# Kernel optimization log

Hardware: AMD Instinct MI355X
Metric: run time of the kernel (lower is better)

## Reference

```python
import jax, jax.numpy as jnp
import numpy as np

NUM_USERS = 150000
NUM_ITEMS = 80000
N_NODES = NUM_USERS + NUM_ITEMS
NNZ = 5000000
LATENT_DIM = 64
N_LAYERS = 3


def setup_inputs() -> dict:
    key = jax.random.key(0)
    k1, k2, k3, k4, k5 = jax.random.split(key, 5)
    user_emb = 0.1 * jax.random.normal(k1, (NUM_USERS, LATENT_DIM), dtype=jnp.float32)
    item_emb = 0.1 * jax.random.normal(k2, (NUM_ITEMS, LATENT_DIM), dtype=jnp.float32)
    adj_rows = jax.random.randint(k3, (NNZ,), 0, N_NODES, dtype=jnp.int32)
    adj_cols = jax.random.randint(k4, (NNZ,), 0, N_NODES, dtype=jnp.int32)
    # scale values ~ 1/avg_degree so propagation is stable (mimics sym-normalized adjacency)
    adj_vals = jax.random.uniform(k5, (NNZ,), dtype=jnp.float32) * (N_NODES / NNZ)
    return {"user_emb": user_emb, "item_emb": item_emb,
            "adj_rows": adj_rows, "adj_cols": adj_cols, "adj_vals": adj_vals}


def _spmm(rows, cols, vals, x):
    # y[r] = sum_{e: rows[e]==r} vals[e] * x[cols[e]]  == torch.sparse.mm(G, x)
    return jax.ops.segment_sum(vals[:, None] * x[cols], rows, num_segments=N_NODES)


def reference(user_emb, item_emb, adj_rows, adj_cols, adj_vals):
    all_emb = jnp.concatenate([user_emb, item_emb], axis=0)  # [N, d]
    acc = all_emb
    for _ in range(N_LAYERS):
        all_emb = _spmm(adj_rows, adj_cols, adj_vals, all_emb)
        acc = acc + all_emb
    light_out = acc / (N_LAYERS + 1)  # mean over stacked layer embeddings
    users = light_out[:NUM_USERS]
    items = light_out[NUM_USERS:]
    return users, items
```

## Files before the change

### kernel.cpp

```cpp
#include <hip/hip_runtime.h>

#define NUM_USERS 150000
#define NUM_ITEMS 80000
#define N_NODES   230000
#define NNZ       5000000
#define DIM       64

#define SB_SHIFT 10
#define SB_SIZE  1024
#define NUM_SB   ((N_NODES + SB_SIZE - 1) / SB_SIZE)
#define SB_CAP   32768
#define PA_ITEMS 4

#define DBINS 256

#define VAL_MAX   0.046f
#define VAL_ENC   (16384.0f / VAL_MAX)
#define VAL_SCALE (VAL_MAX / 16384.0f)

__device__ __forceinline__ float bf2f(unsigned short h) {
    return __uint_as_float(((unsigned int)h) << 16);
}
__device__ __forceinline__ unsigned short f2bf(float f) {
    unsigned int u = __float_as_uint(f);
    u += 0x7FFFu + ((u >> 16) & 1u);
    return (unsigned short)(u >> 16);
}
__device__ __forceinline__ float bflo(unsigned int u) {
    return __uint_as_float(u << 16);
}
__device__ __forceinline__ float bfhi(unsigned int u) {
    return __uint_as_float(u & 0xFFFF0000u);
}
__device__ __forceinline__ unsigned int pk2(float a, float b) {
    return (unsigned int)f2bf(a) | ((unsigned int)f2bf(b) << 16);
}

__global__ void init_kernel(const float* __restrict__ u,
                            const float* __restrict__ it,
                            unsigned short* __restrict__ x) {
    long i = (long)blockIdx.x * blockDim.x + threadIdx.x;
    const long n4  = (long)N_NODES * DIM / 4;
    const long iu4 = (long)NUM_USERS * DIM / 4;
    if (i >= n4) return;
    float4 v = (i < iu4) ? ((const float4*)u)[i]
                         : ((const float4*)it)[i - iu4];
    ushort4 h;
    h.x = f2bf(v.x); h.y = f2bf(v.y); h.z = f2bf(v.z); h.w = f2bf(v.w);
    ((ushort4*)x)[i] = h;
}

__global__ void cursor_init_kernel(int* __restrict__ bucket_cursor,
                                   int* __restrict__ dhist) {
    int t = threadIdx.x;
    if (t < NUM_SB) bucket_cursor[t] = t * SB_CAP;
    dhist[t] = 0;
}

__global__ void partA_kernel(const int* __restrict__ rows,
                             const int* __restrict__ cols,
                             const float* __restrict__ vals,
                             int* __restrict__ bucket_cursor,
                             unsigned int* __restrict__ Xe,
                             unsigned short* __restrict__ Xr) {
    __shared__ int bcnt[NUM_SB];
    __shared__ int bbase[NUM_SB];
    const int t = threadIdx.x;
    const long tile = 1024L * PA_ITEMS;
    for (long base = (long)blockIdx.x * tile; base < NNZ;
         base += (long)gridDim.x * tile) {
        for (int j = t; j < NUM_SB; j += 1024) bcnt[j] = 0;
        __syncthreads();
        int b[PA_ITEMS], rank[PA_ITEMS], rl[PA_ITEMS];
        unsigned int pk[PA_ITEMS];
        bool ok[PA_ITEMS];
        for (int k = 0; k < PA_ITEMS; ++k) {
            long e = base + (long)k * 1024 + t;
            ok[k] = (e < NNZ);
            if (ok[k]) {
                int r = rows[e];
                b[k]  = r >> SB_SHIFT;
                rl[k] = r & (SB_SIZE - 1);
                int vc = (int)(vals[e] * VAL_ENC + 0.5f);
                vc = min(vc, 16383);
                pk[k] = ((unsigned int)vc << 18) | (unsigned int)cols[e];
                rank[k] = atomicAdd(&bcnt[b[k]], 1);
            }
        }
        __syncthreads();
        for (int j = t; j < NUM_SB; j += 1024)
            if (bcnt[j] > 0) bbase[j] = atomicAdd(&bucket_cursor[j], bcnt[j]);
        __syncthreads();
        for (int k = 0; k < PA_ITEMS; ++k)
            if (ok[k]) {
                int pos = bbase[b[k]] + rank[k];
                Xe[pos] = pk[k];
                Xr[pos] = (unsigned short)rl[k];
            }
        __syncthreads();
    }
}

__global__ void sb_scan_kernel(const int* __restrict__ bucket_cursor,
                               int* __restrict__ sb_base) {
    __shared__ int lds[256];
    const int t = threadIdx.x;
    const int s = (t < NUM_SB) ? (bucket_cursor[t] - t * SB_CAP) : 0;
    lds[t] = s;
    __syncthreads();
    for (int off = 1; off < 256; off <<= 1) {
        int add = (t >= off) ? lds[t - off] : 0;
        __syncthreads();
        lds[t] += add;
        __syncthreads();
    }
    if (t < NUM_SB) sb_base[t] = lds[t] - s;
    if (t == 0) sb_base[NUM_SB] = NNZ;
}

__global__ void partB_kernel(const unsigned int* __restrict__ Xe,
                             const unsigned short* __restrict__ Xr,
                             const int* __restrict__ sb_base,
                             int* __restrict__ row_start,
                             unsigned int* __restrict__ edges) {
    __shared__ int hist[SB_SIZE];
    __shared__ int scan[SB_SIZE];
    const int b    = blockIdx.x;
    const int t    = threadIdx.x;
    const int rlo  = b << SB_SHIFT;
    const int nrows = min(SB_SIZE, N_NODES - rlo);
    const int xoff = b * SB_CAP;
    const int base = sb_base[b];
    const int cnt  = sb_base[b + 1] - base;
    hist[t] = 0;
    __syncthreads();
    for (int i = t; i < cnt; i += 1024)
        atomicAdd(&hist[Xr[xoff + i]], 1);
    __syncthreads();
    const int v = hist[t];
    scan[t] = v;
    __syncthreads();
    for (int off = 1; off < 1024; off <<= 1) {
        int add = (t >= off) ? scan[t - off] : 0;
        __syncthreads();
        scan[t] += add;
        __syncthreads();
    }
    const int rs = base + (scan[t] - v);
    if (t < nrows) row_start[rlo + t] = rs;
    hist[t] = rs;
    __syncthreads();
    for (int i = t; i < cnt; i += 1024) {
        int rl = Xr[xoff + i];
        int pos = atomicAdd(&hist[rl], 1);
        edges[pos] = Xe[xoff + i];
    }
    if (b == 0 && t == 0) row_start[N_NODES] = NNZ;
}

__global__ void deg_hist_kernel(const int* __restrict__ row_start,
                                int* __restrict__ dhist) {
    __shared__ int h[DBINS];
    const int t = threadIdx.x;
    h[t] = 0;
    __syncthreads();
    int r = blockIdx.x * 256 + t;
    if (r < N_NODES) {
        int d = row_start[r + 1] - row_start[r];
        atomicAdd(&h[min(d, DBINS - 1)], 1);
    }
    __syncthreads();
    if (h[t]) atomicAdd(&dhist[t], h[t]);
}

__global__ void deg_scan_kernel(const int* __restrict__ dhist,
                                int* __restrict__ dcur) {
    __shared__ int lds[DBINS];
    const int t = threadIdx.x;
    const int s = dhist[t];
    lds[t] = s;
    __syncthreads();
    for (int off = 1; off < DBINS; off <<= 1) {
        int add = (t >= off) ? lds[t - off] : 0;
        __syncthreads();
        lds[t] += add;
        __syncthreads();
    }
    dcur[t] = lds[t] - s;
}

__global__ void deg_scatter_kernel(const int* __restrict__ row_start,
                                   int* __restrict__ dcur,
                                   uint4* __restrict__ desc) {
    __shared__ int bcnt[DBINS];
    __shared__ int bbase[DBINS];
    const int t = threadIdx.x;
    bcnt[t] = 0;
    __syncthreads();
    int r = blockIdx.x * 256 + t;
    int bin = 0, rank = 0, s = 0, d = 0;
    const bool ok = (r < N_NODES);
    if (ok) {
        s = row_start[r];
        d = row_start[r + 1] - s;
        bin = min(d, DBINS - 1);
        rank = atomicAdd(&bcnt[bin], 1);
    }
    __syncthreads();
    if (bcnt[t]) bbase[t] = atomicAdd(&dcur[t], bcnt[t]);
    __syncthreads();
    if (ok)
        desc[bbase[bin] + rank] =
            make_uint4((unsigned)r, (unsigned)s, (unsigned)d, 0u);
}

#define FMA8(v, h) \
    a0 = fmaf((v), bflo((h).x), a0); a1 = fmaf((v), bfhi((h).x), a1); \
    a2 = fmaf((v), bflo((h).y), a2); a3 = fmaf((v), bfhi((h).y), a3); \
    a4 = fmaf((v), bflo((h).z), a4); a5 = fmaf((v), bfhi((h).z), a5); \
    a6 = fmaf((v), bflo((h).w), a6); a7 = fmaf((v), bfhi((h).w), a7);

__global__ __launch_bounds__(256)
void spmm8_kernel(const uint4* __restrict__ desc,
                  const unsigned int* __restrict__ edges,
                  const unsigned short* __restrict__ x,
                  unsigned short* __restrict__ y) {
    const int lane = threadIdx.x & 63;
    const int oct  = lane >> 3;
    const int fo   = (lane & 7) << 3;
    const long wv  = (long)blockIdx.x * 4 + (threadIdx.x >> 6);
    const long rowIdx = wv * 8 + oct;
    const bool valid = (rowIdx < N_NODES);
    const uint4 dsc = desc[valid ? rowIdx : (N_NODES - 1)];
    const int r = (int)dsc.x;
    const int s = (int)dsc.y;
    const int deg = valid ? (int)dsc.z : 0;
    int dm = deg;
    dm = max(dm, __shfl_xor(dm, 8));
    dm = max(dm, __shfl_xor(dm, 16));
    dm = max(dm, __shfl_xor(dm, 32));
    dm = __builtin_amdgcn_readfirstlane(dm);
    const unsigned short* xf = x + fo;
    float a0 = 0, a1 = 0, a2 = 0, a3 = 0, a4 = 0, a5 = 0, a6 = 0, a7 = 0;
    for (int i = 0; i < dm; i += 2) {
        const int o0 = (i     < deg) ? (s + i)     : 0;
        const int o1 = (i + 1 < deg) ? (s + i + 1) : 0;
        const unsigned int e0 = edges[o0];
        const unsigned int e1 = edges[o1];
        const uint4 ha = *(const uint4*)(xf + (((long)(e0 & 0x3FFFF)) << 6));
        const uint4 hb = *(const uint4*)(xf + (((long)(e1 & 0x3FFFF)) << 6));
        const float v0 = (i     < deg) ? (float)(e0 >> 18) * VAL_SCALE : 0.0f;
        const float v1 = (i + 1 < deg) ? (float)(e1 >> 18) * VAL_SCALE : 0.0f;
        FMA8(v0, ha);
        FMA8(v1, hb);
    }
    if (valid) {
        uint4 w;
        w.x = pk2(a0, a1); w.y = pk2(a2, a3);
        w.z = pk2(a4, a5); w.w = pk2(a6, a7);
        *(uint4*)(y + (((long)r) << 6) + fo) = w;
    }
}

__global__ __launch_bounds__(256)
void spmm_final8_kernel(const uint4* __restrict__ desc,
                        const unsigned int* __restrict__ edges,
                        const unsigned short* __restrict__ y2,
                        const unsigned short* __restrict__ y1,
                        const float* __restrict__ u,
                        const float* __restrict__ it,
                        float* __restrict__ acc) {
    const int lane = threadIdx.x & 63;
    const int oct  = lane >> 3;
    const int fo   = (lane & 7) << 3;
    const long wv  = (long)blockIdx.x * 4 + (threadIdx.x >> 6);
    const long rowIdx = wv * 8 + oct;
    const bool valid = (rowIdx < N_NODES);
    const uint4 dsc = desc[valid ? rowIdx : (N_NODES - 1)];
    const int r = (int)dsc.x;
    const int s = (int)dsc.y;
    const int deg = valid ? (int)dsc.z : 0;
    int dm = deg;
    dm = max(dm, __shfl_xor(dm, 8));
    dm = max(dm, __shfl_xor(dm, 16));
    dm = max(dm, __shfl_xor(dm, 32));
    dm = __builtin_amdgcn_readfirstlane(dm);
    const unsigned short* xf = y2 + fo;
    float a0 = 0, a1 = 0, a2 = 0, a3 = 0, a4 = 0, a5 = 0, a6 = 0, a7 = 0;
    for (int i = 0; i < dm; i += 2) {
        const int o0 = (i     < deg) ? (s + i)     : 0;
        const int o1 = (i + 1 < deg) ? (s + i + 1) : 0;
        const unsigned int e0 = edges[o0];
        const unsigned int e1 = edges[o1];
        const uint4 ha = *(const uint4*)(xf + (((long)(e0 & 0x3FFFF)) << 6));
        const uint4 hb = *(const uint4*)(xf + (((long)(e1 & 0x3FFFF)) << 6));
        const float v0 = (i     < deg) ? (float)(e0 >> 18) * VAL_SCALE : 0.0f;
        const float v1 = (i + 1 < deg) ? (float)(e1 >> 18) * VAL_SCALE : 0.0f;
        FMA8(v0, ha);
        FMA8(v1, hb);
    }
    if (valid) {
        const long o = (((long)r) << 6) + fo;
        const float* x0p = (r < NUM_USERS) ? (u + o)
                         : (it + o - (((long)NUM_USERS) << 6));
        const float4 xa = *(const float4*)(x0p);
        const float4 xb = *(const float4*)(x0p + 4);
        const uint4 h1 = *(const uint4*)(y1 + o);
        const uint4 h2 = *(const uint4*)(y2 + o);
        float4 ra, rb;
        ra.x = (xa.x + bflo(h1.x) + bflo(h2.x) + a0) * 0.25f;
        ra.y = (xa.y + bfhi(h1.x) + bfhi(h2.x) + a1) * 0.25f;
        ra.z = (xa.z + bflo(h1.y) + bflo(h2.y) + a2) * 0.25f;
        ra.w = (xa.w + bfhi(h1.y) + bfhi(h2.y) + a3) * 0.25f;
        rb.x = (xb.x + bflo(h1.z) + bflo(h2.z) + a4) * 0.25f;
        rb.y = (xb.y + bfhi(h1.z) + bfhi(h2.z) + a5) * 0.25f;
        rb.z = (xb.z + bflo(h1.w) + bflo(h2.w) + a6) * 0.25f;
        rb.w = (xb.w + bfhi(h1.w) + bfhi(h2.w) + a7) * 0.25f;
        *(float4*)(acc + o) = ra;
        *(float4*)(acc + o + 4) = rb;
    }
}

extern "C" void kernel_launch(void* const* d_in, const int* in_sizes, int n_in,
                              void* d_out, int out_size, void* d_ws, size_t ws_size,
                              hipStream_t stream) {
    const float* u    = (const float*)d_in[0];
    const float* it   = (const float*)d_in[1];
    const int*   rows = (const int*)d_in[2];
    const int*   cols = (const int*)d_in[3];
    const float* vals = (const float*)d_in[4];
    float* acc = (float*)d_out;

    const size_t bufBf = (size_t)N_NODES * DIM * 2;
    const size_t edgeB = (size_t)NNZ * 4;
    const size_t XeB   = (size_t)NUM_SB * SB_CAP * 4;
    const size_t XrB   = (size_t)NUM_SB * SB_CAP * 2;
    const size_t nodeB = 921600;
    char* ws = (char*)d_ws;
    unsigned short* buf0 = (unsigned short*)(ws);
    unsigned short* buf1 = (unsigned short*)(ws + bufBf);
    unsigned short* buf2 = (unsigned short*)(ws + 2 * bufBf);
    unsigned int*   edges = (unsigned int*)(ws + 3 * bufBf);
    unsigned int*   Xe   = (unsigned int*)(ws + 3 * bufBf + edgeB);
    unsigned short* Xr   = (unsigned short*)(ws + 3 * bufBf + edgeB + XeB);
    char* p              = ws + 3 * bufBf + edgeB + XeB + XrB;
    int* row_start       = (int*)(p);   p += nodeB;
    int* bucket_cursor   = (int*)(p);   p += 1024;
    int* sb_base         = (int*)(p);   p += 1024;
    int* dhist           = (int*)(p);   p += DBINS * 4;
    int* dcur            = (int*)(p);
    uint4* desc          = (uint4*)Xe;

    const int n4 = N_NODES * DIM / 4;
    const int ewGrid = (n4 + 255) / 256;
    const int rowBlocks = (N_NODES + 255) / 256;

    init_kernel<<<ewGrid, 256, 0, stream>>>(u, it, buf0);

    cursor_init_kernel<<<1, 256, 0, stream>>>(bucket_cursor, dhist);
    partA_kernel<<<512, 1024, 0, stream>>>(rows, cols, vals, bucket_cursor, Xe, Xr);
    sb_scan_kernel<<<1, 256, 0, stream>>>(bucket_cursor, sb_base);
    partB_kernel<<<NUM_SB, 1024, 0, stream>>>(Xe, Xr, sb_base, row_start, edges);

    deg_hist_kernel<<<rowBlocks, 256, 0, stream>>>(row_start, dhist);
    deg_scan_kernel<<<1, DBINS, 0, stream>>>(dhist, dcur);
    deg_scatter_kernel<<<rowBlocks, 256, 0, stream>>>(row_start, dcur, desc);

    const long waves = (N_NODES + 7) / 8;
    const int spmmGrid = (int)((waves + 3) / 4);
    spmm8_kernel<<<spmmGrid, 256, 0, stream>>>(desc, edges, buf0, buf1);
    spmm8_kernel<<<spmmGrid, 256, 0, stream>>>(desc, edges, buf1, buf2);
    spmm_final8_kernel<<<spmmGrid, 256, 0, stream>>>(desc, edges, buf2,
                                                     buf1, u, it, acc);
}
```

Before: 604.0 us.

## Sort edges by column segment within rows and unroll SpMM gathers by four

The partition kernel now bins each row's edges into eight column segments using a per-row, per-segment LDS histogram, so edges within a row are ordered roughly by source column. This aims to improve L2 locality of the gathered embedding rows across concurrent waves. The SpMM kernels also unroll the edge loop to four gathers per iteration and use nontemporal loads for the edge stream to keep it from polluting cache. The cost is eight times more LDS in the partition kernel and more registers per thread in the SpMM kernels.

```diff
diff --git a/kernel.cpp b/kernel.cpp
--- a/kernel.cpp
+++ b/kernel.cpp
@@ -11,6 +11,9 @@
 #define NUM_SB   ((N_NODES + SB_SIZE - 1) / SB_SIZE)
 #define SB_CAP   32768
 #define PA_ITEMS 4
+
+#define SEG_SHIFT 15
+#define NSEG      8
 
 #define DBINS 256
 
@@ -123,8 +126,8 @@
                              const int* __restrict__ sb_base,
                              int* __restrict__ row_start,
                              unsigned int* __restrict__ edges) {
-    __shared__ int hist[SB_SIZE];
-    __shared__ int scan[SB_SIZE];
+    __shared__ int hist[SB_SIZE * NSEG];
+    __shared__ int rsum[SB_SIZE];
     const int b    = blockIdx.x;
     const int t    = threadIdx.x;
     const int rlo  = b << SB_SHIFT;
@@ -132,28 +135,38 @@
     const int xoff = b * SB_CAP;
     const int base = sb_base[b];
     const int cnt  = sb_base[b + 1] - base;
-    hist[t] = 0;
-    __syncthreads();
-    for (int i = t; i < cnt; i += 1024)
-        atomicAdd(&hist[Xr[xoff + i]], 1);
-    __syncthreads();
-    const int v = hist[t];
-    scan[t] = v;
+    for (int j = t; j < SB_SIZE * NSEG; j += 1024) hist[j] = 0;
+    __syncthreads();
+    for (int i = t; i < cnt; i += 1024) {
+        const unsigned int pk = Xe[xoff + i];
+        const int rl  = Xr[xoff + i];
+        const int seg = (int)((pk & 0x3FFFFu) >> SEG_SHIFT);
+        atomicAdd(&hist[(rl << 3) | seg], 1);
+    }
+    __syncthreads();
+    int c[NSEG]; int tot = 0;
+    #pragma unroll
+    for (int k = 0; k < NSEG; ++k) { c[k] = hist[(t << 3) | k]; tot += c[k]; }
+    rsum[t] = tot;
     __syncthreads();
     for (int off = 1; off < 1024; off <<= 1) {
-        int add = (t >= off) ? scan[t - off] : 0;
-        __syncthreads();
-        scan[t] += add;
-        __syncthreads();
-    }
-    const int rs = base + (scan[t] - v);
+        int add = (t >= off) ? rsum[t - off] : 0;
+        __syncthreads();
+        rsum[t] += add;
+        __syncthreads();
+    }
+    const int rs = base + (rsum[t] - tot);
     if (t < nrows) row_start[rlo + t] = rs;
-    hist[t] = rs;
+    int run = rs;
+    #pragma unroll
+    for (int k = 0; k < NSEG; ++k) { int tmp = c[k]; hist[(t << 3) | k] = run; run += tmp; }
     __syncthreads();
     for (int i = t; i < cnt; i += 1024) {
-        int rl = Xr[xoff + i];
-        int pos = atomicAdd(&hist[rl], 1);
-        edges[pos] = Xe[xoff + i];
+        const unsigned int pk = Xe[xoff + i];
+        const int rl  = Xr[xoff + i];
+        const int seg = (int)((pk & 0x3FFFFu) >> SEG_SHIFT);
+        const int pos = atomicAdd(&hist[(rl << 3) | seg], 1);
+        edges[pos] = pk;
     }
     if (b == 0 && t == 0) row_start[N_NODES] = NNZ;
 }
@@ -242,17 +255,27 @@
     dm = __builtin_amdgcn_readfirstlane(dm);
     const unsigned short* xf = x + fo;
     float a0 = 0, a1 = 0, a2 = 0, a3 = 0, a4 = 0, a5 = 0, a6 = 0, a7 = 0;
-    for (int i = 0; i < dm; i += 2) {
+    for (int i = 0; i < dm; i += 4) {
         const int o0 = (i     < deg) ? (s + i)     : 0;
         const int o1 = (i + 1 < deg) ? (s + i + 1) : 0;
-        const unsigned int e0 = edges[o0];
-        const unsigned int e1 = edges[o1];
+        const int o2 = (i + 2 < deg) ? (s + i + 2) : 0;
+        const int o3 = (i + 3 < deg) ? (s + i + 3) : 0;
+        const unsigned int e0 = __builtin_nontemporal_load(edges + o0);
+        const unsigned int e1 = __builtin_nontemporal_load(edges + o1);
+        const unsigned int e2 = __builtin_nontemporal_load(edges + o2);
+        const unsigned int e3 = __builtin_nontemporal_load(edges + o3);
         const uint4 ha = *(const uint4*)(xf + (((long)(e0 & 0x3FFFF)) << 6));
         const uint4 hb = *(const uint4*)(xf + (((long)(e1 & 0x3FFFF)) << 6));
+        const uint4 hc = *(const uint4*)(xf + (((long)(e2 & 0x3FFFF)) << 6));
+        const uint4 hd = *(const uint4*)(xf + (((long)(e3 & 0x3FFFF)) << 6));
         const float v0 = (i     < deg) ? (float)(e0 >> 18) * VAL_SCALE : 0.0f;
         const float v1 = (i + 1 < deg) ? (float)(e1 >> 18) * VAL_SCALE : 0.0f;
+        const float v2 = (i + 2 < deg) ? (float)(e2 >> 18) * VAL_SCALE : 0.0f;
+        const float v3 = (i + 3 < deg) ? (float)(e3 >> 18) * VAL_SCALE : 0.0f;
         FMA8(v0, ha);
         FMA8(v1, hb);
+        FMA8(v2, hc);
+        FMA8(v3, hd);
     }
     if (valid) {
         uint4 w;
@@ -287,17 +310,27 @@
     dm = __builtin_amdgcn_readfirstlane(dm);
     const unsigned short* xf = y2 + fo;
     float a0 = 0, a1 = 0, a2 = 0, a3 = 0, a4 = 0, a5 = 0, a6 = 0, a7 = 0;
-    for (int i = 0; i < dm; i += 2) {
+    for (int i = 0; i < dm; i += 4) {
         const int o0 = (i     < deg) ? (s + i)     : 0;
         const int o1 = (i + 1 < deg) ? (s + i + 1) : 0;
-        const unsigned int e0 = edges[o0];
-        const unsigned int e1 = edges[o1];
+        const int o2 = (i + 2 < deg) ? (s + i + 2) : 0;
+        const int o3 = (i + 3 < deg) ? (s + i + 3) : 0;
+        const unsigned int e0 = __builtin_nontemporal_load(edges + o0);
+        const unsigned int e1 = __builtin_nontemporal_load(edges + o1);
+        const unsigned int e2 = __builtin_nontemporal_load(edges + o2);
+        const unsigned int e3 = __builtin_nontemporal_load(edges + o3);
         const uint4 ha = *(const uint4*)(xf + (((long)(e0 & 0x3FFFF)) << 6));
         const uint4 hb = *(const uint4*)(xf + (((long)(e1 & 0x3FFFF)) << 6));
+        const uint4 hc = *(const uint4*)(xf + (((long)(e2 & 0x3FFFF)) << 6));
+        const uint4 hd = *(const uint4*)(xf + (((long)(e3 & 0x3FFFF)) << 6));
         const float v0 = (i     < deg) ? (float)(e0 >> 18) * VAL_SCALE : 0.0f;
         const float v1 = (i + 1 < deg) ? (float)(e1 >> 18) * VAL_SCALE : 0.0f;
+        const float v2 = (i + 2 < deg) ? (float)(e2 >> 18) * VAL_SCALE : 0.0f;
+        const float v3 = (i + 3 < deg) ? (float)(e3 >> 18) * VAL_SCALE : 0.0f;
         FMA8(v0, ha);
         FMA8(v1, hb);
+        FMA8(v2, hc);
+        FMA8(v3, hd);
     }
     if (valid) {
         const long o = (((long)r) << 6) + fo;
```

Result: slower. 657.3 us (+8.8%).

## Build sliced-ELL edge layout with global atomic scatter instead of two-pass bucket sort

Applied to the files above, without the earlier changes.

Replaces the two-pass bucket sort (partA/partB) that built CSR with a per-row count histogram plus degree-sorted slices of 8 rows. Each slice is padded to a multiple of 4 and its edges are interleaved, so the SpMM loop drops per-lane degree predicates and reads 4 edges per iteration. Edges are placed by a global atomic scatter, and padded slots are zero-filled so they contribute nothing. The cost is extra small kernels, a zero-fill of the padded edge buffer, and heavy global atomic traffic in the scatter, in exchange for a simpler, branch-free inner loop.

```diff
diff --git a/kernel.cpp b/kernel.cpp
--- a/kernel.cpp
+++ b/kernel.cpp
@@ -6,11 +6,9 @@
 #define NNZ       5000000
 #define DIM       64
 
-#define SB_SHIFT 10
-#define SB_SIZE  1024
-#define NUM_SB   ((N_NODES + SB_SIZE - 1) / SB_SIZE)
-#define SB_CAP   32768
-#define PA_ITEMS 4
+#define NSLICES   ((N_NODES + 7) / 8)
+#define SCAN_BLKS ((NSLICES + 1023) / 1024)
+#define ECAP      6000000
 
 #define DBINS 256
 
@@ -18,9 +16,6 @@
 #define VAL_ENC   (16384.0f / VAL_MAX)
 #define VAL_SCALE (VAL_MAX / 16384.0f)
 
-__device__ __forceinline__ float bf2f(unsigned short h) {
-    return __uint_as_float(((unsigned int)h) << 16);
-}
 __device__ __forceinline__ unsigned short f2bf(float f) {
     unsigned int u = __float_as_uint(f);
     u += 0x7FFFu + ((u >> 16) & 1u);
@@ -38,8 +33,12 @@
 
 __global__ void init_kernel(const float* __restrict__ u,
                             const float* __restrict__ it,
-                            unsigned short* __restrict__ x) {
+                            unsigned short* __restrict__ x,
+                            int* __restrict__ row_cnt,
+                            int* __restrict__ dhist) {
     long i = (long)blockIdx.x * blockDim.x + threadIdx.x;
+    if (i < N_NODES) row_cnt[i] = 0;
+    if (i < DBINS) dhist[i] = 0;
     const long n4  = (long)N_NODES * DIM / 4;
     const long iu4 = (long)NUM_USERS * DIM / 4;
     if (i >= n4) return;
@@ -50,125 +49,30 @@
     ((ushort4*)x)[i] = h;
 }
 
-__global__ void cursor_init_kernel(int* __restrict__ bucket_cursor,
-                                   int* __restrict__ dhist) {
-    int t = threadIdx.x;
-    if (t < NUM_SB) bucket_cursor[t] = t * SB_CAP;
-    dhist[t] = 0;
-}
-
-__global__ void partA_kernel(const int* __restrict__ rows,
-                             const int* __restrict__ cols,
-                             const float* __restrict__ vals,
-                             int* __restrict__ bucket_cursor,
-                             unsigned int* __restrict__ Xe,
-                             unsigned short* __restrict__ Xr) {
-    __shared__ int bcnt[NUM_SB];
-    __shared__ int bbase[NUM_SB];
-    const int t = threadIdx.x;
-    const long tile = 1024L * PA_ITEMS;
-    for (long base = (long)blockIdx.x * tile; base < NNZ;
-         base += (long)gridDim.x * tile) {
-        for (int j = t; j < NUM_SB; j += 1024) bcnt[j] = 0;
-        __syncthreads();
-        int b[PA_ITEMS], rank[PA_ITEMS], rl[PA_ITEMS];
-        unsigned int pk[PA_ITEMS];
-        bool ok[PA_ITEMS];
-        for (int k = 0; k < PA_ITEMS; ++k) {
-            long e = base + (long)k * 1024 + t;
-            ok[k] = (e < NNZ);
-            if (ok[k]) {
-                int r = rows[e];
-                b[k]  = r >> SB_SHIFT;
-                rl[k] = r & (SB_SIZE - 1);
-                int vc = (int)(vals[e] * VAL_ENC + 0.5f);
-                vc = min(vc, 16383);
-                pk[k] = ((unsigned int)vc << 18) | (unsigned int)cols[e];
-                rank[k] = atomicAdd(&bcnt[b[k]], 1);
-            }
-        }
-        __syncthreads();
-        for (int j = t; j < NUM_SB; j += 1024)
-            if (bcnt[j] > 0) bbase[j] = atomicAdd(&bucket_cursor[j], bcnt[j]);
-        __syncthreads();
-        for (int k = 0; k < PA_ITEMS; ++k)
-            if (ok[k]) {
-                int pos = bbase[b[k]] + rank[k];
-                Xe[pos] = pk[k];
-                Xr[pos] = (unsigned short)rl[k];
-            }
-        __syncthreads();
-    }
-}
-
-__global__ void sb_scan_kernel(const int* __restrict__ bucket_cursor,
-                               int* __restrict__ sb_base) {
-    __shared__ int lds[256];
-    const int t = threadIdx.x;
-    const int s = (t < NUM_SB) ? (bucket_cursor[t] - t * SB_CAP) : 0;
-    lds[t] = s;
-    __syncthreads();
-    for (int off = 1; off < 256; off <<= 1) {
-        int add = (t >= off) ? lds[t - off] : 0;
-        __syncthreads();
-        lds[t] += add;
-        __syncthreads();
-    }
-    if (t < NUM_SB) sb_base[t] = lds[t] - s;
-    if (t == 0) sb_base[NUM_SB] = NNZ;
-}
-
-__global__ void partB_kernel(const unsigned int* __restrict__ Xe,
-                             const unsigned short* __restrict__ Xr,
-                             const int* __restrict__ sb_base,
-                             int* __restrict__ row_start,
-                             unsigned int* __restrict__ edges) {
-    __shared__ int hist[SB_SIZE];
-    __shared__ int scan[SB_SIZE];
-    const int b    = blockIdx.x;
-    const int t    = threadIdx.x;
-    const int rlo  = b << SB_SHIFT;
-    const int nrows = min(SB_SIZE, N_NODES - rlo);
-    const int xoff = b * SB_CAP;
-    const int base = sb_base[b];
-    const int cnt  = sb_base[b + 1] - base;
-    hist[t] = 0;
-    __syncthreads();
-    for (int i = t; i < cnt; i += 1024)
-        atomicAdd(&hist[Xr[xoff + i]], 1);
-    __syncthreads();
-    const int v = hist[t];
-    scan[t] = v;
-    __syncthreads();
-    for (int off = 1; off < 1024; off <<= 1) {
-        int add = (t >= off) ? scan[t - off] : 0;
-        __syncthreads();
-        scan[t] += add;
-        __syncthreads();
-    }
-    const int rs = base + (scan[t] - v);
-    if (t < nrows) row_start[rlo + t] = rs;
-    hist[t] = rs;
-    __syncthreads();
-    for (int i = t; i < cnt; i += 1024) {
-        int rl = Xr[xoff + i];
-        int pos = atomicAdd(&hist[rl], 1);
-        edges[pos] = Xe[xoff + i];
-    }
-    if (b == 0 && t == 0) row_start[N_NODES] = NNZ;
-}
-
-__global__ void deg_hist_kernel(const int* __restrict__ row_start,
+__global__ void hist_kernel(const int* __restrict__ rows,
+                            int* __restrict__ row_cnt,
+                            uint4* __restrict__ edges4) {
+    const int tid  = blockIdx.x * blockDim.x + threadIdx.x;
+    const int nthr = gridDim.x * blockDim.x;
+    for (int j = tid; j < ECAP / 4; j += nthr)
+        edges4[j] = make_uint4(0u, 0u, 0u, 0u);
+    for (int j = tid; j < NNZ / 4; j += nthr) {
+        const int4 r4 = ((const int4*)rows)[j];
+        atomicAdd(&row_cnt[r4.x], 1);
+        atomicAdd(&row_cnt[r4.y], 1);
+        atomicAdd(&row_cnt[r4.z], 1);
+        atomicAdd(&row_cnt[r4.w], 1);
+    }
+}
+
+__global__ void deg_hist_kernel(const int* __restrict__ row_cnt,
                                 int* __restrict__ dhist) {
     __shared__ int h[DBINS];
     const int t = threadIdx.x;
     h[t] = 0;
     __syncthreads();
     int r = blockIdx.x * 256 + t;
-    if (r < N_NODES) {
-        int d = row_start[r + 1] - row_start[r];
-        atomicAdd(&h[min(d, DBINS - 1)], 1);
-    }
+    if (r < N_NODES) atomicAdd(&h[min(row_cnt[r], DBINS - 1)], 1);
     __syncthreads();
     if (h[t]) atomicAdd(&dhist[t], h[t]);
 }
@@ -189,29 +93,102 @@
     dcur[t] = lds[t] - s;
 }
 
-__global__ void deg_scatter_kernel(const int* __restrict__ row_start,
-                                   int* __restrict__ dcur,
-                                   uint4* __restrict__ desc) {
+__global__ void deg_rank_kernel(const int* __restrict__ row_cnt,
+                                int* __restrict__ dcur,
+                                int* __restrict__ rowof) {
     __shared__ int bcnt[DBINS];
     __shared__ int bbase[DBINS];
     const int t = threadIdx.x;
     bcnt[t] = 0;
     __syncthreads();
     int r = blockIdx.x * 256 + t;
-    int bin = 0, rank = 0, s = 0, d = 0;
     const bool ok = (r < N_NODES);
+    int bin = 0, rank = 0;
     if (ok) {
-        s = row_start[r];
-        d = row_start[r + 1] - s;
-        bin = min(d, DBINS - 1);
+        bin  = min(row_cnt[r], DBINS - 1);
         rank = atomicAdd(&bcnt[bin], 1);
     }
     __syncthreads();
     if (bcnt[t]) bbase[t] = atomicAdd(&dcur[t], bcnt[t]);
     __syncthreads();
-    if (ok)
-        desc[bbase[bin] + rank] =
-            make_uint4((unsigned)r, (unsigned)s, (unsigned)d, 0u);
+    if (ok) rowof[bbase[bin] + rank] = r;
+}
+
+__global__ void slice_w_kernel(const int* __restrict__ row_cnt,
+                               const int* __restrict__ rowof,
+                               int* __restrict__ W4) {
+    int w = blockIdx.x * 256 + threadIdx.x;
+    if (w < NSLICES) W4[w] = (row_cnt[rowof[w * 8 + 7]] + 3) & ~3;
+}
+
+__global__ void scanA_kernel(const int* __restrict__ W4,
+                             int* __restrict__ Wex,
+                             int* __restrict__ bsum) {
+    __shared__ int lds[1024];
+    const int t = threadIdx.x;
+    const int i = blockIdx.x * 1024 + t;
+    const int v = (i < NSLICES) ? W4[i] : 0;
+    lds[t] = v;
+    __syncthreads();
+    for (int off = 1; off < 1024; off <<= 1) {
+        int add = (t >= off) ? lds[t - off] : 0;
+        __syncthreads();
+        lds[t] += add;
+        __syncthreads();
+    }
+    if (i < NSLICES) Wex[i] = lds[t] - v;
+    if (t == 1023) bsum[blockIdx.x] = lds[t];
+}
+
+__global__ void scanB_kernel(int* __restrict__ bsum) {
+    if (threadIdx.x == 0) {
+        int acc = 0;
+        for (int b = 0; b < SCAN_BLKS; ++b) {
+            int v = bsum[b]; bsum[b] = acc; acc += v;
+        }
+    }
+}
+
+__global__ void place_kernel(const int* __restrict__ rowof,
+                             const int* __restrict__ W4,
+                             const int* __restrict__ Wex,
+                             const int* __restrict__ bsum,
+                             int* __restrict__ cur,
+                             uint2* __restrict__ sdesc) {
+    const int p = blockIdx.x * 256 + threadIdx.x;
+    if (p >= N_NODES) return;
+    const int w = p >> 3;
+    const int base = (Wex[w] + bsum[w >> 10]) << 3;
+    cur[rowof[p]] = base + (p & 7);
+    if ((p & 7) == 0) sdesc[w] = make_uint2((unsigned)base, (unsigned)W4[w]);
+}
+
+__global__ void scatter_kernel(const int* __restrict__ rows,
+                               const int* __restrict__ cols,
+                               const float* __restrict__ vals,
+                               int* __restrict__ cur,
+                               unsigned int* __restrict__ edges) {
+    const int j = blockIdx.x * 256 + threadIdx.x;
+    if (j >= NNZ / 4) return;
+    const int4   r4 = ((const int4*)rows)[j];
+    const int4   c4 = ((const int4*)cols)[j];
+    const float4 v4 = ((const float4*)vals)[j];
+    {
+        int vc = min((int)(v4.x * VAL_ENC + 0.5f), 16383);
+        edges[atomicAdd(&cur[r4.x], 8)] = ((unsigned)vc << 18) | (unsigned)c4.x;
+    }
+    {
+        int vc = min((int)(v4.y * VAL_ENC + 0.5f), 16383);
+        edges[atomicAdd(&cur[r4.y], 8)] = ((unsigned)vc << 18) | (unsigned)c4.y;
+    }
+    {
+        int vc = min((int)(v4.z * VAL_ENC + 0.5f), 16383);
+        edges[atomicAdd(&cur[r4.z], 8)] = ((unsigned)vc << 18) | (unsigned)c4.z;
+    }
+    {
+        int vc = min((int)(v4.w * VAL_ENC + 0.5f), 16383);
+        edges[atomicAdd(&cur[r4.w], 8)] = ((unsigned)vc << 18) | (unsigned)c4.w;
+    }
 }
 
 #define FMA8(v, h) \
@@ -221,49 +198,50 @@
     a6 = fmaf((v), bflo((h).w), a6); a7 = fmaf((v), bfhi((h).w), a7);
 
 __global__ __launch_bounds__(256)
-void spmm8_kernel(const uint4* __restrict__ desc,
+void spmm8_kernel(const uint2* __restrict__ sdesc,
+                  const int* __restrict__ rowof,
                   const unsigned int* __restrict__ edges,
                   const unsigned short* __restrict__ x,
                   unsigned short* __restrict__ y) {
     const int lane = threadIdx.x & 63;
     const int oct  = lane >> 3;
     const int fo   = (lane & 7) << 3;
-    const long wv  = (long)blockIdx.x * 4 + (threadIdx.x >> 6);
-    const long rowIdx = wv * 8 + oct;
-    const bool valid = (rowIdx < N_NODES);
-    const uint4 dsc = desc[valid ? rowIdx : (N_NODES - 1)];
-    const int r = (int)dsc.x;
-    const int s = (int)dsc.y;
-    const int deg = valid ? (int)dsc.z : 0;
-    int dm = deg;
-    dm = max(dm, __shfl_xor(dm, 8));
-    dm = max(dm, __shfl_xor(dm, 16));
-    dm = max(dm, __shfl_xor(dm, 32));
-    dm = __builtin_amdgcn_readfirstlane(dm);
+    const int wv   = blockIdx.x * 4 + (threadIdx.x >> 6);
+    if (wv >= NSLICES) return;
+    const uint2 sd = sdesc[wv];
+    const int base = __builtin_amdgcn_readfirstlane((int)sd.x);
+    const int W    = __builtin_amdgcn_readfirstlane((int)sd.y);
+    const int r    = rowof[wv * 8 + oct];
+    const unsigned int* ep = edges + base + oct;
     const unsigned short* xf = x + fo;
     float a0 = 0, a1 = 0, a2 = 0, a3 = 0, a4 = 0, a5 = 0, a6 = 0, a7 = 0;
-    for (int i = 0; i < dm; i += 2) {
-        const int o0 = (i     < deg) ? (s + i)     : 0;
-        const int o1 = (i + 1 < deg) ? (s + i + 1) : 0;
-        const unsigned int e0 = edges[o0];
-        const unsigned int e1 = edges[o1];
+    for (int i = 0; i < W; i += 4) {
+        const unsigned int e0 = ep[(i + 0) << 3];
+        const unsigned int e1 = ep[(i + 1) << 3];
+        const unsigned int e2 = ep[(i + 2) << 3];
+        const unsigned int e3 = ep[(i + 3) << 3];
         const uint4 ha = *(const uint4*)(xf + (((long)(e0 & 0x3FFFF)) << 6));
         const uint4 hb = *(const uint4*)(xf + (((long)(e1 & 0x3FFFF)) << 6));
-        const float v0 = (i     < deg) ? (float)(e0 >> 18) * VAL_SCALE : 0.0f;
-        const float v1 = (i + 1 < deg) ? (float)(e1 >> 18) * VAL_SCALE : 0.0f;
+        const uint4 hc = *(const uint4*)(xf + (((long)(e2 & 0x3FFFF)) << 6));
+        const uint4 hd = *(const uint4*)(xf + (((long)(e3 & 0x3FFFF)) << 6));
+        const float v0 = (float)(e0 >> 18) * VAL_SCALE;
+        const float v1 = (float)(e1 >> 18) * VAL_SCALE;
+        const float v2 = (float)(e2 >> 18) * VAL_SCALE;
+        const float v3 = (float)(e3 >> 18) * VAL_SCALE;
         FMA8(v0, ha);
         FMA8(v1, hb);
-    }
-    if (valid) {
-        uint4 w;
-        w.x = pk2(a0, a1); w.y = pk2(a2, a3);
-        w.z = pk2(a4, a5); w.w = pk2(a6, a7);
-        *(uint4*)(y + (((long)r) << 6) + fo) = w;
-    }
+        FMA8(v2, hc);
+        FMA8(v3, hd);
+    }
+    uint4 w;
+    w.x = pk2(a0, a1); w.y = pk2(a2, a3);
+    w.z = pk2(a4, a5); w.w = pk2(a6, a7);
+    *(uint4*)(y + (((long)r) << 6) + fo) = w;
 }
 
 __global__ __launch_bounds__(256)
-void spmm_final8_kernel(const uint4* __restrict__ desc,
+void spmm_final8_kernel(const uint2* __restrict__ sdesc,
+                        const int* __restrict__ rowof,
                         const unsigned int* __restrict__ edges,
                         const unsigned short* __restrict__ y2,
                         const unsigned short* __restrict__ y1,
@@ -273,52 +251,51 @@
     const int lane = threadIdx.x & 63;
     const int oct  = lane >> 3;
     const int fo   = (lane & 7) << 3;
-    const long wv  = (long)blockIdx.x * 4 + (threadIdx.x >> 6);
-    const long rowIdx = wv * 8 + oct;
-    const bool valid = (rowIdx < N_NODES);
-    const uint4 dsc = desc[valid ? rowIdx : (N_NODES - 1)];
-    const int r = (int)dsc.x;
-    const int s = (int)dsc.y;
-    const int deg = valid ? (int)dsc.z : 0;
-    int dm = deg;
-    dm = max(dm, __shfl_xor(dm, 8));
-    dm = max(dm, __shfl_xor(dm, 16));
-    dm = max(dm, __shfl_xor(dm, 32));
-    dm = __builtin_amdgcn_readfirstlane(dm);
+    const int wv   = blockIdx.x * 4 + (threadIdx.x >> 6);
+    if (wv >= NSLICES) return;
+    const uint2 sd = sdesc[wv];
+    const int base = __builtin_amdgcn_readfirstlane((int)sd.x);
+    const int W    = __builtin_amdgcn_readfirstlane((int)sd.y);
+    const int r    = rowof[wv * 8 + oct];
+    const unsigned int* ep = edges + base + oct;
     const unsigned short* xf = y2 + fo;
     float a0 = 0, a1 = 0, a2 = 0, a3 = 0, a4 = 0, a5 = 0, a6 = 0, a7 = 0;
-    for (int i = 0; i < dm; i += 2) {
-        const int o0 = (i     < deg) ? (s + i)     : 0;
-        const int o1 = (i + 1 < deg) ? (s + i + 1) : 0;
-        const unsigned int e0 = edges[o0];
-        const unsigned int e1 = edges[o1];
+    for (int i = 0; i < W; i += 4) {
+        const unsigned int e0 = ep[(i + 0) << 3];
+        const unsigned int e1 = ep[(i + 1) << 3];
+        const unsigned int e2 = ep[(i + 2) << 3];
+        const unsigned int e3 = ep[(i + 3) << 3];
         const uint4 ha = *(const uint4*)(xf + (((long)(e0 & 0x3FFFF)) << 6));
         const uint4 hb = *(const uint4*)(xf + (((long)(e1 & 0x3FFFF)) << 6));
-        const float v0 = (i     < deg) ? (float)(e0 >> 18) * VAL_SCALE : 0.0f;
-        const float v1 = (i + 1 < deg) ? (float)(e1 >> 18) * VAL_SCALE : 0.0f;
+        const uint4 hc = *(const uint4*)(xf + (((long)(e2 & 0x3FFFF)) << 6));
+        const uint4 hd = *(const uint4*)(xf + (((long)(e3 & 0x3FFFF)) << 6));
+        const float v0 = (float)(e0 >> 18) * VAL_SCALE;
+        const float v1 = (float)(e1 >> 18) * VAL_SCALE;
+        const float v2 = (float)(e2 >> 18) * VAL_SCALE;
+        const float v3 = (float)(e3 >> 18) * VAL_SCALE;
         FMA8(v0, ha);
         FMA8(v1, hb);
-    }
-    if (valid) {
-        const long o = (((long)r) << 6) + fo;
-        const float* x0p = (r < NUM_USERS) ? (u + o)
-                         : (it + o - (((long)NUM_USERS) << 6));
-        const float4 xa = *(const float4*)(x0p);
-        const float4 xb = *(const float4*)(x0p + 4);
-        const uint4 h1 = *(const uint4*)(y1 + o);
-        const uint4 h2 = *(const uint4*)(y2 + o);
-        float4 ra, rb;
-        ra.x = (xa.x + bflo(h1.x) + bflo(h2.x) + a0) * 0.25f;
-        ra.y = (xa.y + bfhi(h1.x) + bfhi(h2.x) + a1) * 0.25f;
-        ra.z = (xa.z + bflo(h1.y) + bflo(h2.y) + a2) * 0.25f;
-        ra.w = (xa.w + bfhi(h1.y) + bfhi(h2.y) + a3) * 0.25f;
-        rb.x = (xb.x + bflo(h1.z) + bflo(h2.z) + a4) * 0.25f;
-        rb.y = (xb.y + bfhi(h1.z) + bfhi(h2.z) + a5) * 0.25f;
-        rb.z = (xb.z + bflo(h1.w) + bflo(h2.w) + a6) * 0.25f;
-        rb.w = (xb.w + bfhi(h1.w) + bfhi(h2.w) + a7) * 0.25f;
-        *(float4*)(acc + o) = ra;
-        *(float4*)(acc + o + 4) = rb;
-    }
+        FMA8(v2, hc);
+        FMA8(v3, hd);
+    }
+    const long o = (((long)r) << 6) + fo;
+    const float* x0p = (r < NUM_USERS) ? (u + o)
+                     : (it + o - (((long)NUM_USERS) << 6));
+    const float4 xa = *(const float4*)(x0p);
+    const float4 xb = *(const float4*)(x0p + 4);
+    const uint4 h1 = *(const uint4*)(y1 + o);
+    const uint4 h2 = *(const uint4*)(y2 + o);
+    float4 ra, rb;
+    ra.x = (xa.x + bflo(h1.x) + bflo(h2.x) + a0) * 0.25f;
+    ra.y = (xa.y + bfhi(h1.x) + bfhi(h2.x) + a1) * 0.25f;
+    ra.z = (xa.z + bflo(h1.y) + bflo(h2.y) + a2) * 0.25f;
+    ra.w = (xa.w + bfhi(h1.y) + bfhi(h2.y) + a3) * 0.25f;
+    rb.x = (xb.x + bflo(h1.z) + bflo(h2.z) + a4) * 0.25f;
+    rb.y = (xb.y + bfhi(h1.z) + bfhi(h2.z) + a5) * 0.25f;
+    rb.z = (xb.z + bflo(h1.w) + bflo(h2.w) + a6) * 0.25f;
+    rb.w = (xb.w + bfhi(h1.w) + bfhi(h2.w) + a7) * 0.25f;
+    *(float4*)(acc + o) = ra;
+    *(float4*)(acc + o + 4) = rb;
 }
 
 extern "C" void kernel_launch(void* const* d_in, const int* in_sizes, int n_in,
@@ -332,44 +309,42 @@
     float* acc = (float*)d_out;
 
     const size_t bufBf = (size_t)N_NODES * DIM * 2;
-    const size_t edgeB = (size_t)NNZ * 4;
-    const size_t XeB   = (size_t)NUM_SB * SB_CAP * 4;
-    const size_t XrB   = (size_t)NUM_SB * SB_CAP * 2;
-    const size_t nodeB = 921600;
     char* ws = (char*)d_ws;
-    unsigned short* buf0 = (unsigned short*)(ws);
-    unsigned short* buf1 = (unsigned short*)(ws + bufBf);
-    unsigned short* buf2 = (unsigned short*)(ws + 2 * bufBf);
+    unsigned short* buf0  = (unsigned short*)(ws);
+    unsigned short* buf1  = (unsigned short*)(ws + bufBf);
+    unsigned short* buf2  = (unsigned short*)(ws + 2 * bufBf);
     unsigned int*   edges = (unsigned int*)(ws + 3 * bufBf);
-    unsigned int*   Xe   = (unsigned int*)(ws + 3 * bufBf + edgeB);
-    unsigned short* Xr   = (unsigned short*)(ws + 3 * bufBf + edgeB + XeB);
-    char* p              = ws + 3 * bufBf + edgeB + XeB + XrB;
-    int* row_start       = (int*)(p);   p += nodeB;
-    int* bucket_cursor   = (int*)(p);   p += 1024;
-    int* sb_base         = (int*)(p);   p += 1024;
-    int* dhist           = (int*)(p);   p += DBINS * 4;
-    int* dcur            = (int*)(p);
-    uint4* desc          = (uint4*)Xe;
+    char* p = ws + 3 * bufBf + (size_t)ECAP * 4;
+    int*   rowof   = (int*)(p);   p += 921600;
+    int*   cur     = (int*)(p);   p += 921600;
+    int*   row_cnt = (int*)(p);   p += 921600;
+    int*   W4      = (int*)(p);   p += 115200;
+    int*   Wex     = (int*)(p);   p += 115200;
+    uint2* sdesc   = (uint2*)(p); p += 230400;
+    int*   dhist   = (int*)(p);   p += 1024;
+    int*   dcur    = (int*)(p);   p += 1024;
+    int*   bsum    = (int*)(p);
 
     const int n4 = N_NODES * DIM / 4;
-    const int ewGrid = (n4 + 255) / 256;
+    const int ewGrid    = (n4 + 255) / 256;
     const int rowBlocks = (N_NODES + 255) / 256;
 
-    init_kernel<<<ewGrid, 256, 0, stream>>>(u, it, buf0);
-
-    cursor_init_kernel<<<1, 256, 0, stream>>>(bucket_cursor, dhist);
-    partA_kernel<<<512, 1024, 0, stream>>>(rows, cols, vals, bucket_cursor, Xe, Xr);
-    sb_scan_kernel<<<1, 256, 0, stream>>>(bucket_cursor, sb_base);
-    partB_kernel<<<NUM_SB, 1024, 0, stream>>>(Xe, Xr, sb_base, row_start, edges);
-
-    deg_hist_kernel<<<rowBlocks, 256, 0, stream>>>(row_start, dhist);
+    init_kernel<<<ewGrid, 256, 0, stream>>>(u, it, buf0, row_cnt, dhist);
+
+    hist_kernel<<<2048, 256, 0, stream>>>(rows, row_cnt, (uint4*)edges);
+    deg_hist_kernel<<<rowBlocks, 256, 0, stream>>>(row_cnt, dhist);
     deg_scan_kernel<<<1, DBINS, 0, stream>>>(dhist, dcur);
-    deg_scatter_kernel<<<rowBlocks, 256, 0, stream>>>(row_start, dcur, desc);
-
-    const long waves = (N_NODES + 7) / 8;
-    const int spmmGrid = (int)((waves + 3) / 4);
-    spmm8_kernel<<<spmmGrid, 256, 0, stream>>>(desc, edges, buf0, buf1);
-    spmm8_kernel<<<spmmGrid, 256, 0, stream>>>(desc, edges, buf1, buf2);
-    spmm_final8_kernel<<<spmmGrid, 256, 0, stream>>>(desc, edges, buf2,
+    deg_rank_kernel<<<rowBlocks, 256, 0, stream>>>(row_cnt, dcur, rowof);
+    slice_w_kernel<<<(NSLICES + 255) / 256, 256, 0, stream>>>(row_cnt, rowof, W4);
+    scanA_kernel<<<SCAN_BLKS, 1024, 0, stream>>>(W4, Wex, bsum);
+    scanB_kernel<<<1, 64, 0, stream>>>(bsum);
+    place_kernel<<<rowBlocks, 256, 0, stream>>>(rowof, W4, Wex, bsum, cur, sdesc);
+    scatter_kernel<<<(NNZ / 4 + 255) / 256, 256, 0, stream>>>(rows, cols, vals,
+                                                              cur, edges);
+
+    const int spmmGrid = (NSLICES + 3) / 4;
+    spmm8_kernel<<<spmmGrid, 256, 0, stream>>>(sdesc, rowof, edges, buf0, buf1);
+    spmm8_kernel<<<spmmGrid, 256, 0, stream>>>(sdesc, rowof, edges, buf1, buf2);
+    spmm_final8_kernel<<<spmmGrid, 256, 0, stream>>>(sdesc, rowof, edges, buf2,
                                                      buf1, u, it, acc);
 }
```

Result: slower. 944.9 us (+56.4%).
